# Performance work log

Measured on AMD Instinct MI355X. Metric: run time of the kernel, lower is better.

The kernel has to match this reference:

```python
import jax, jax.numpy as jnp
import numpy as np

B, C, T = 8, 128, 32768
OUT, K, DIL = 128, 2, 2


def dilated_indices(T, k, d):
    # Faithful vectorized version of the original Python double loop:
    # idx[span*k + j] = span + j*d, clamped to T (the zero-pad slot) when >= T+1.
    padded = T + 1
    idx = jnp.arange(padded)[:, None] + jnp.arange(k)[None, :] * d  # (padded, k)
    idx = idx.reshape(-1)                                           # (k*padded,)
    return jnp.where(idx >= padded, T, idx)


def setup_inputs() -> dict:
    key = jax.random.key(0)
    k1, k2, k3 = jax.random.split(key, 3)
    x = jax.random.normal(k1, (B, C, T), dtype=jnp.float32)
    # Conv1d(in=C, out=OUT, kernel_size=K) parameters
    W = jax.random.normal(k2, (OUT, C, K), dtype=jnp.float32) * 0.05
    b = jax.random.normal(k3, (OUT,), dtype=jnp.float32) * 0.05
    return {"x": x, "W": W, "b": b}


def reference(x, W, b):
    Bx, Cx, Tx = x.shape
    # pad one zero column at the end of the time axis (torch.cat with zeros)
    xp = jnp.concatenate([x, jnp.zeros((Bx, Cx, 1), x.dtype)], axis=2)  # (B,C,T+1)
    idx = dilated_indices(Tx, K, DIL)                                   # (K*(T+1),)
    swizzle = xp[:, :, idx]                                             # (B,C,K*(T+1))
    # Conv1d with stride == kernel_size over the swizzled buffer is a GEMM
    # over non-overlapping windows of size K.
    sw = swizzle.reshape(Bx, Cx, Tx + 1, K)                             # (B,C,T+1,K)
    out = jnp.einsum('bcpk,ock->bop', sw, W) + b[None, :, None]         # (B,OUT,T+1)
    return out
```

## Files before the change

kernel.cpp:

```cpp
#include <hip/hip_runtime.h>


namespace {

constexpr int kC   = 128;
constexpr int kT   = 32768;
constexpr int kP   = kT + 1;
constexpr int kOut = 128;
constexpr int kNP  = 128;
constexpr int kTilesPerB = kT / kNP;
constexpr int kUnitsPerBlock = 4;
constexpr int kNBlocks = 512;
constexpr int kLStride = 136;
constexpr int kLBuf    = 130 * kLStride;

typedef __attribute__((ext_vector_type(8))) short short8;
typedef __attribute__((ext_vector_type(4))) float f32x4;

__device__ __forceinline__ short f2bf(float f) {
    unsigned int u = __builtin_bit_cast(unsigned int, f);
    u += 0x7fffu + ((u >> 16) & 1u);
    return (short)(u >> 16);
}

__device__ __forceinline__ int lds_idx(int pos, int c) {
    return pos * kLStride + (c ^ (((pos >> 2) & 7) << 3));
}

__device__ __forceinline__ void lds_barrier() {
    asm volatile("s_waitcnt lgkmcnt(0)" ::: "memory");
    __builtin_amdgcn_s_barrier();
}

struct StageRegs {
    f32x4 m[16];
    float h[8];
};

__device__ __forceinline__ void stage_issue(const float* __restrict__ xb, int p0,
                                            int tid, StageRegs& r) {
    const int pgrp = tid & 31;
    const int cgrp = tid >> 5;
    const float* col = xb + p0 + pgrp * 4;
    #pragma unroll
    for (int j = 0; j < 16; ++j) {
        r.m[j] = *reinterpret_cast<const f32x4*>(col + ((size_t)(cgrp * 16 + j) << 15));
    }
    if (tid < 32) {
        const int gph = p0 + 128 + (tid & 1);
        const float* colh = xb + (gph < kT ? gph : 0);
        const int c0 = (tid >> 1) * 8;
        #pragma unroll
        for (int j = 0; j < 8; ++j) r.h[j] = colh[(size_t)(c0 + j) << 15];
    }
}

__device__ __forceinline__ void stage_commit(short* __restrict__ xs, int p0,
                                             int tid, const StageRegs& r) {
    const int pgrp = tid & 31;
    const int cgrp = tid >> 5;
    #pragma unroll
    for (int i = 0; i < 4; ++i) {
        const int pos = pgrp * 4 + i;
        #pragma unroll
        for (int h = 0; h < 2; ++h) {
            short8 v;
            #pragma unroll
            for (int j = 0; j < 8; ++j) v[j] = f2bf(r.m[h * 8 + j][i]);
            *reinterpret_cast<short8*>(xs + lds_idx(pos, cgrp * 16 + h * 8)) = v;
        }
    }
    if (tid < 32) {
        const int pos = 128 + (tid & 1);
        const bool okh = (p0 + pos) < kT;
        const int c0 = (tid >> 1) * 8;
        short8 v;
        #pragma unroll
        for (int j = 0; j < 8; ++j) v[j] = okh ? f2bf(r.h[j]) : (short)0;
        *reinterpret_cast<short8*>(xs + lds_idx(pos, c0)) = v;
    }
}

__global__ __launch_bounds__(256, 2) void dconv_mfma(
    const float* __restrict__ x, const float* __restrict__ W,
    const float* __restrict__ bias, float* __restrict__ out)
{
    __shared__ __align__(16) short xs[2][kLBuf];

    const int tid  = threadIdx.x;
    const int lane = tid & 63;
    const int wv   = tid >> 6;
    const int blk  = blockIdx.x;
    const int u0   = blk * kUnitsPerBlock;
    const int bb   = u0 >> 8;
    const int t0   = u0 & 255;

    if (blk < 8 && tid < kOut) {
        out[(size_t)blk * kOut * kP + (size_t)tid * kP + kT] = bias[tid];
    }

    const int rowbase = wv * 32;
    short8 wf[2][2][4];
    #pragma unroll
    for (int cc = 0; cc < 2; ++cc) {
        const int o = rowbase + cc * 16 + (lane & 15);
        #pragma unroll
        for (int s = 0; s < 4; ++s) {
            const int cb = s * 32 + (lane >> 4) * 8;
            const f32x4* wp = reinterpret_cast<const f32x4*>(W + o * (kC * 2) + cb * 2);
            f32x4 wr[4];
            #pragma unroll
            for (int q = 0; q < 4; ++q) wr[q] = wp[q];
            short8 f0, f1;
            #pragma unroll
            for (int q = 0; q < 4; ++q) {
                f0[q * 2 + 0] = f2bf(wr[q][0]);  f1[q * 2 + 0] = f2bf(wr[q][1]);
                f0[q * 2 + 1] = f2bf(wr[q][2]);  f1[q * 2 + 1] = f2bf(wr[q][3]);
            }
            wf[0][cc][s] = f0;
            wf[1][cc][s] = f1;
        }
    }
    const float bv0 = bias[rowbase + (lane & 15)];
    const float bv1 = bias[rowbase + 16 + (lane & 15)];

    const float* xb = x + (size_t)bb * kC * kT;
    float* ob = out + (size_t)bb * kOut * kP;

    StageRegs r;
    stage_issue(xb, t0 << 7, tid, r);
    stage_commit(xs[0], t0 << 7, tid, r);
    stage_issue(xb, (t0 + 1) << 7, tid, r);
    lds_barrier();

    #pragma unroll 1
    for (int i = 0; i < kUnitsPerBlock; ++i) {
        const short* cur = xs[i & 1];
        const int p0 = (t0 + i) << 7;

        f32x4 acc[2][8];
        #pragma unroll
        for (int nc = 0; nc < 8; ++nc) {
            #pragma unroll
            for (int rr = 0; rr < 4; ++rr) { acc[0][nc][rr] = bv0; acc[1][nc][rr] = bv1; }
        }
        #pragma unroll
        for (int tap = 0; tap < 2; ++tap) {
            #pragma unroll
            for (int s = 0; s < 4; ++s) {
                const int cb = s * 32 + (lane >> 4) * 8;
                #pragma unroll
                for (int nc = 0; nc < 8; ++nc) {
                    const int pos = nc * 16 + (lane & 15) + 2 * tap;
                    const short8 xf = *reinterpret_cast<const short8*>(cur + lds_idx(pos, cb));
                    acc[0][nc] = __builtin_amdgcn_mfma_f32_16x16x32_bf16(xf, wf[tap][0][s], acc[0][nc], 0, 0, 0);
                    acc[1][nc] = __builtin_amdgcn_mfma_f32_16x16x32_bf16(xf, wf[tap][1][s], acc[1][nc], 0, 0, 0);
                }
            }
        }

        if (i + 1 < kUnitsPerBlock) {
            stage_commit(xs[(i + 1) & 1], (t0 + i + 1) << 7, tid, r);
        }

        {
            const int o0   = rowbase + (lane & 15);
            const int prow = (lane >> 4) * 4;
            #pragma unroll
            for (int nc = 0; nc < 8; ++nc) {
                const int p = p0 + nc * 16 + prow;
                #pragma unroll
                for (int cc = 0; cc < 2; ++cc) {
                    __builtin_memcpy(ob + (size_t)(o0 + cc * 16) * kP + p, &acc[cc][nc],
                                     sizeof(f32x4));
                }
            }
        }

        if (i + 2 < kUnitsPerBlock) {
            stage_issue(xb, (t0 + i + 2) << 7, tid, r);
        }

        if (i + 1 < kUnitsPerBlock) lds_barrier();
    }
}

}

extern "C" void kernel_launch(void* const* d_in, const int* in_sizes, int n_in,
                              void* d_out, int out_size, void* d_ws, size_t ws_size,
                              hipStream_t stream) {
    const float* x    = (const float*)d_in[0];
    const float* W    = (const float*)d_in[1];
    const float* bias = (const float*)d_in[2];
    float* out        = (float*)d_out;

    dim3 grid(kNBlocks);
    dim3 block(256);
    hipLaunchKernelGGL(dconv_mfma, grid, block, 0, stream, x, W, bias, out);
}
```

Baseline: 305.6 us.

## Stage input tiles via direct global-to-LDS DMA with 64-position tiles

Replaces the register-staged global loads with global_load_lds DMA into an fp32 LDS staging buffer, then converts each tile to bf16 in LDS before the MFMA loop. Tiles shrink from 128 to 64 positions with 8 tiles per block, and a rotated write pattern avoids bank conflicts during conversion. The aim is to free the VGPRs that held staged data and overlap the next tile's DMA with compute. The cost is an extra LDS round trip and barrier per tile, and the bf16 buffer is now single-buffered.

```diff
diff --git a/kernel.cpp b/kernel.cpp
--- a/kernel.cpp
+++ b/kernel.cpp
@@ -7,14 +7,16 @@
 constexpr int kT   = 32768;
 constexpr int kP   = kT + 1;
 constexpr int kOut = 128;
-constexpr int kNP  = 128;
-constexpr int kTilesPerB = kT / kNP;
-constexpr int kUnitsPerBlock = 4;
+constexpr int kNP  = 64;
+constexpr int kTilesPerBatch = kT / kNP;
+constexpr int kTPB = 8;
 constexpr int kNBlocks = 512;
 constexpr int kLStride = 136;
-constexpr int kLBuf    = 130 * kLStride;
+constexpr int kF32Main = 128 * 64;
+constexpr int kF32Halo = 128 * 4;
 
 typedef __attribute__((ext_vector_type(8))) short short8;
+typedef __attribute__((ext_vector_type(4))) short s16x4;
 typedef __attribute__((ext_vector_type(4))) float f32x4;
 
 __device__ __forceinline__ short f2bf(float f) {
@@ -23,61 +25,74 @@
     return (short)(u >> 16);
 }
 
-__device__ __forceinline__ int lds_idx(int pos, int c) {
-    return pos * kLStride + (c ^ (((pos >> 2) & 7) << 3));
-}
-
+__device__ __forceinline__ void dma16(const float* g, float* l) {
+    __builtin_amdgcn_global_load_lds(
+        (const __attribute__((address_space(1))) void*)g,
+        (__attribute__((address_space(3))) void*)l,
+        16, 0, 0);
+}
+
+__device__ __forceinline__ void wait_vm0_barrier() {
+    asm volatile("s_waitcnt vmcnt(0)" ::: "memory");
+    __builtin_amdgcn_s_barrier();
+}
 __device__ __forceinline__ void lds_barrier() {
     asm volatile("s_waitcnt lgkmcnt(0)" ::: "memory");
     __builtin_amdgcn_s_barrier();
 }
 
-struct StageRegs {
-    f32x4 m[16];
-    float h[8];
-};
-
-__device__ __forceinline__ void stage_issue(const float* __restrict__ xb, int p0,
-                                            int tid, StageRegs& r) {
-    const int pgrp = tid & 31;
-    const int cgrp = tid >> 5;
-    const float* col = xb + p0 + pgrp * 4;
+__device__ __forceinline__ void stage_dma(const float* __restrict__ xb, int p0,
+                                          int wv, int lane, float* __restrict__ xf,
+                                          bool lastTile) {
+    const int q = lane >> 4;
+    const int s = lane & 15;
     #pragma unroll
-    for (int j = 0; j < 16; ++j) {
-        r.m[j] = *reinterpret_cast<const f32x4*>(col + ((size_t)(cgrp * 16 + j) << 15));
-    }
-    if (tid < 32) {
-        const int gph = p0 + 128 + (tid & 1);
-        const float* colh = xb + (gph < kT ? gph : 0);
-        const int c0 = (tid >> 1) * 8;
-        #pragma unroll
-        for (int j = 0; j < 8; ++j) r.h[j] = colh[(size_t)(c0 + j) << 15];
-    }
-}
-
-__device__ __forceinline__ void stage_commit(short* __restrict__ xs, int p0,
-                                             int tid, const StageRegs& r) {
-    const int pgrp = tid & 31;
-    const int cgrp = tid >> 5;
+    for (int jj = 0; jj < 8; ++jj) {
+        const int j  = wv * 8 + jj;
+        const int c  = 4 * j + q;
+        const int pw = (s - j) & 15;
+        dma16(xb + (size_t)c * kT + p0 + pw * 4, xf + j * 256);
+    }
+    if (wv == 0) {
+        #pragma unroll
+        for (int h = 0; h < 2; ++h) {
+            const int c  = 64 * h + lane;
+            const int gp = p0 + kNP;
+            dma16(xb + (size_t)c * kT + (lastTile ? p0 : gp),
+                  xf + kF32Main + h * 256);
+        }
+    }
+}
+
+__device__ __forceinline__ void convert_tile(const float* __restrict__ xf,
+                                             short* __restrict__ xs,
+                                             int tid, bool lastTile) {
+    const int cg = tid & 31;
+    const int c0 = cg * 4;
+    const int ph = tid >> 5;
     #pragma unroll
-    for (int i = 0; i < 4; ++i) {
-        const int pos = pgrp * 4 + i;
-        #pragma unroll
-        for (int h = 0; h < 2; ++h) {
-            short8 v;
-            #pragma unroll
-            for (int j = 0; j < 8; ++j) v[j] = f2bf(r.m[h * 8 + j][i]);
-            *reinterpret_cast<short8*>(xs + lds_idx(pos, cgrp * 16 + h * 8)) = v;
-        }
-    }
-    if (tid < 32) {
-        const int pos = 128 + (tid & 1);
-        const bool okh = (p0 + pos) < kT;
-        const int c0 = (tid >> 1) * 8;
-        short8 v;
-        #pragma unroll
-        for (int j = 0; j < 8; ++j) v[j] = okh ? f2bf(r.h[j]) : (short)0;
-        *reinterpret_cast<short8*>(xs + lds_idx(pos, c0)) = v;
+    for (int u = 0; u < 2; ++u) {
+        const int pw   = ph * 2 + u;
+        const int slot = (pw + cg) & 15;
+        f32x4 g[4];
+        #pragma unroll
+        for (int r = 0; r < 4; ++r) {
+            g[r] = *reinterpret_cast<const f32x4*>(xf + (c0 + r) * 64 + slot * 4);
+        }
+        #pragma unroll
+        for (int i = 0; i < 4; ++i) {
+            const int pos = pw * 4 + i;
+            s16x4 v;
+            v[0] = f2bf(g[0][i]); v[1] = f2bf(g[1][i]);
+            v[2] = f2bf(g[2][i]); v[3] = f2bf(g[3][i]);
+            *reinterpret_cast<s16x4*>(xs + pos * kLStride + c0) = v;
+        }
+    }
+    if (tid < 128) {
+        const int c = tid;
+        const f32x4 hh = *reinterpret_cast<const f32x4*>(xf + kF32Main + c * 4);
+        xs[64 * kLStride + c] = lastTile ? (short)0 : f2bf(hh[0]);
+        xs[65 * kLStride + c] = lastTile ? (short)0 : f2bf(hh[1]);
     }
 }
 
@@ -85,19 +100,24 @@
     const float* __restrict__ x, const float* __restrict__ W,
     const float* __restrict__ bias, float* __restrict__ out)
 {
-    __shared__ __align__(16) short xs[2][kLBuf];
+    __shared__ __align__(16) float xf[kF32Main + kF32Halo];
+    __shared__ __align__(16) short xs[66 * kLStride];
 
     const int tid  = threadIdx.x;
     const int lane = tid & 63;
     const int wv   = tid >> 6;
     const int blk  = blockIdx.x;
-    const int u0   = blk * kUnitsPerBlock;
-    const int bb   = u0 >> 8;
-    const int t0   = u0 & 255;
+    const int bb   = blk >> 6;
+    const int t0   = (blk & 63) * kTPB;
+
+    const float* xb = x + (size_t)bb * kC * kT;
+    float* ob = out + (size_t)bb * kOut * kP;
 
     if (blk < 8 && tid < kOut) {
         out[(size_t)blk * kOut * kP + (size_t)tid * kP + kT] = bias[tid];
     }
+
+    stage_dma(xb, t0 * kNP, wv, lane, xf, false);
 
     const int rowbase = wv * 32;
     short8 wf[2][2][4];
@@ -124,23 +144,24 @@
     const float bv0 = bias[rowbase + (lane & 15)];
     const float bv1 = bias[rowbase + 16 + (lane & 15)];
 
-    const float* xb = x + (size_t)bb * kC * kT;
-    float* ob = out + (size_t)bb * kOut * kP;
-
-    StageRegs r;
-    stage_issue(xb, t0 << 7, tid, r);
-    stage_commit(xs[0], t0 << 7, tid, r);
-    stage_issue(xb, (t0 + 1) << 7, tid, r);
-    lds_barrier();
+    wait_vm0_barrier();
 
     #pragma unroll 1
-    for (int i = 0; i < kUnitsPerBlock; ++i) {
-        const short* cur = xs[i & 1];
-        const int p0 = (t0 + i) << 7;
-
-        f32x4 acc[2][8];
-        #pragma unroll
-        for (int nc = 0; nc < 8; ++nc) {
+    for (int i = 0; i < kTPB; ++i) {
+        const int p0 = (t0 + i) * kNP;
+        const bool lastTile = (t0 + i) == (kTilesPerBatch - 1);
+
+        convert_tile(xf, xs, tid, lastTile);
+        lds_barrier();
+
+        if (i + 1 < kTPB) {
+            stage_dma(xb, (t0 + i + 1) * kNP, wv, lane, xf,
+                      (t0 + i + 1) == (kTilesPerBatch - 1));
+        }
+
+        f32x4 acc[2][4];
+        #pragma unroll
+        for (int nc = 0; nc < 4; ++nc) {
             #pragma unroll
             for (int rr = 0; rr < 4; ++rr) { acc[0][nc][rr] = bv0; acc[1][nc][rr] = bv1; }
         }
@@ -150,24 +171,20 @@
             for (int s = 0; s < 4; ++s) {
                 const int cb = s * 32 + (lane >> 4) * 8;
                 #pragma unroll
-                for (int nc = 0; nc < 8; ++nc) {
+                for (int nc = 0; nc < 4; ++nc) {
                     const int pos = nc * 16 + (lane & 15) + 2 * tap;
-                    const short8 xf = *reinterpret_cast<const short8*>(cur + lds_idx(pos, cb));
-                    acc[0][nc] = __builtin_amdgcn_mfma_f32_16x16x32_bf16(xf, wf[tap][0][s], acc[0][nc], 0, 0, 0);
-                    acc[1][nc] = __builtin_amdgcn_mfma_f32_16x16x32_bf16(xf, wf[tap][1][s], acc[1][nc], 0, 0, 0);
+                    const short8 xfrag = *reinterpret_cast<const short8*>(xs + pos * kLStride + cb);
+                    acc[0][nc] = __builtin_amdgcn_mfma_f32_16x16x32_bf16(xfrag, wf[tap][0][s], acc[0][nc], 0, 0, 0);
+                    acc[1][nc] = __builtin_amdgcn_mfma_f32_16x16x32_bf16(xfrag, wf[tap][1][s], acc[1][nc], 0, 0, 0);
                 }
             }
-        }
-
-        if (i + 1 < kUnitsPerBlock) {
-            stage_commit(xs[(i + 1) & 1], (t0 + i + 1) << 7, tid, r);
         }
 
         {
             const int o0   = rowbase + (lane & 15);
             const int prow = (lane >> 4) * 4;
             #pragma unroll
-            for (int nc = 0; nc < 8; ++nc) {
+            for (int nc = 0; nc < 4; ++nc) {
                 const int p = p0 + nc * 16 + prow;
                 #pragma unroll
                 for (int cc = 0; cc < 2; ++cc) {
@@ -177,11 +194,7 @@
             }
         }
 
-        if (i + 2 < kUnitsPerBlock) {
-            stage_issue(xb, (t0 + i + 2) << 7, tid, r);
-        }
-
-        if (i + 1 < kUnitsPerBlock) lds_barrier();
+        if (i + 1 < kTPB) wait_vm0_barrier();
     }
 }
 
```

Measured after the change: 290.2 us. 5.0% less time.

## Stage input via async global-to-LDS DMA ring and widen tiles to 256 positions

Applied to the files above, without the earlier changes.

Replaces the register-staged input load with global_load_lds DMA into a four-slot fp32 ring buffer of 16-channel chunks, kept three chunks ahead. Each chunk is then converted to bf16 in a single LDS tile. Blocks grow to 512 threads over 256-position tiles, with 8 waves split into 2 output groups by 4 position groups, and there are 256 blocks each doing 4 strided tiles. The goal is to cut VGPR pressure from staging and to overlap HBM reads with conversion. The cost is two barriers per chunk, serialized conversion and compute with no compute overlap within a tile, and a vmcnt(0) drain at the end of each tile.

```diff
diff --git a/kernel.cpp b/kernel.cpp
--- a/kernel.cpp
+++ b/kernel.cpp
@@ -7,12 +7,16 @@
 constexpr int kT   = 32768;
 constexpr int kP   = kT + 1;
 constexpr int kOut = 128;
-constexpr int kNP  = 128;
-constexpr int kTilesPerB = kT / kNP;
-constexpr int kUnitsPerBlock = 4;
-constexpr int kNBlocks = 512;
-constexpr int kLStride = 136;
-constexpr int kLBuf    = 130 * kLStride;
+constexpr int kTileP  = 256;
+constexpr int kTPB    = 4;
+constexpr int kGroups = 32;
+constexpr int kNBlocks = 8 * kGroups;
+constexpr int kChunks = 8;
+constexpr int kQ      = kTPB * kChunks;
+constexpr int kRowF   = 260;
+constexpr int kBufF   = 16 * kRowF + 64;
+constexpr int kPitch  = 136;
+constexpr int kXSRows = kTileP + 2;
 
 typedef __attribute__((ext_vector_type(8))) short short8;
 typedef __attribute__((ext_vector_type(4))) float f32x4;
@@ -23,90 +27,92 @@
     return (short)(u >> 16);
 }
 
-__device__ __forceinline__ int lds_idx(int pos, int c) {
-    return pos * kLStride + (c ^ (((pos >> 2) & 7) << 3));
-}
-
-__device__ __forceinline__ void lds_barrier() {
-    asm volatile("s_waitcnt lgkmcnt(0)" ::: "memory");
-    __builtin_amdgcn_s_barrier();
-}
-
-struct StageRegs {
-    f32x4 m[16];
-    float h[8];
-};
-
-__device__ __forceinline__ void stage_issue(const float* __restrict__ xb, int p0,
-                                            int tid, StageRegs& r) {
-    const int pgrp = tid & 31;
-    const int cgrp = tid >> 5;
-    const float* col = xb + p0 + pgrp * 4;
-    #pragma unroll
-    for (int j = 0; j < 16; ++j) {
-        r.m[j] = *reinterpret_cast<const f32x4*>(col + ((size_t)(cgrp * 16 + j) << 15));
-    }
-    if (tid < 32) {
-        const int gph = p0 + 128 + (tid & 1);
-        const float* colh = xb + (gph < kT ? gph : 0);
-        const int c0 = (tid >> 1) * 8;
-        #pragma unroll
-        for (int j = 0; j < 8; ++j) r.h[j] = colh[(size_t)(c0 + j) << 15];
-    }
-}
-
-__device__ __forceinline__ void stage_commit(short* __restrict__ xs, int p0,
-                                             int tid, const StageRegs& r) {
-    const int pgrp = tid & 31;
-    const int cgrp = tid >> 5;
-    #pragma unroll
-    for (int i = 0; i < 4; ++i) {
-        const int pos = pgrp * 4 + i;
-        #pragma unroll
-        for (int h = 0; h < 2; ++h) {
-            short8 v;
-            #pragma unroll
-            for (int j = 0; j < 8; ++j) v[j] = f2bf(r.m[h * 8 + j][i]);
-            *reinterpret_cast<short8*>(xs + lds_idx(pos, cgrp * 16 + h * 8)) = v;
-        }
-    }
-    if (tid < 32) {
-        const int pos = 128 + (tid & 1);
-        const bool okh = (p0 + pos) < kT;
-        const int c0 = (tid >> 1) * 8;
-        short8 v;
-        #pragma unroll
-        for (int j = 0; j < 8; ++j) v[j] = okh ? f2bf(r.h[j]) : (short)0;
-        *reinterpret_cast<short8*>(xs + lds_idx(pos, c0)) = v;
-    }
-}
-
-__global__ __launch_bounds__(256, 2) void dconv_mfma(
+__device__ __forceinline__ void dma16(const float* g, float* l) {
+    __builtin_amdgcn_global_load_lds(
+        (const __attribute__((address_space(1))) void*)g,
+        (__attribute__((address_space(3))) void*)l, 16, 0, 0);
+}
+__device__ __forceinline__ void dma4(const float* g, float* l) {
+    __builtin_amdgcn_global_load_lds(
+        (const __attribute__((address_space(1))) void*)g,
+        (__attribute__((address_space(3))) void*)l, 4, 0, 0);
+}
+
+__device__ __forceinline__ void issue_chunk(const float* __restrict__ xb, int p0,
+                                            int ch, float* __restrict__ buf,
+                                            int wv, int lane, bool last) {
+    #pragma unroll
+    for (int rr = 0; rr < 2; ++rr) {
+        const int r = 2 * wv + rr;
+        const int c = ch * 16 + r;
+        dma16(xb + (size_t)c * kT + p0 + lane * 4, buf + r * kRowF);
+    }
+    if (wv == 7) {
+        const int hc = ch * 16 + (lane >> 2);
+        const int hp = last ? p0 : (p0 + kTileP);
+        dma4(xb + (size_t)hc * kT + hp + (lane & 3), buf + 16 * kRowF);
+    }
+}
+
+__device__ __forceinline__ void convert_chunk(const float* __restrict__ buf,
+                                              short* __restrict__ xs,
+                                              int ch, int tid, bool last) {
+    const int c  = tid & 15;
+    const int pq = tid >> 4;
+    const int cc = ch * 16 + c;
+    #pragma unroll
+    for (int half = 0; half < 2; ++half) {
+        const int q = pq + half * 32;
+        const f32x4 v = *reinterpret_cast<const f32x4*>(buf + c * kRowF + q * 4);
+        #pragma unroll
+        for (int i = 0; i < 4; ++i) {
+            xs[(q * 4 + i) * kPitch + cc] = f2bf(v[i]);
+        }
+    }
+    if (tid < 16) {
+        const float h0 = buf[16 * kRowF + tid * 4 + 0];
+        const float h1 = buf[16 * kRowF + tid * 4 + 1];
+        xs[256 * kPitch + ch * 16 + tid] = last ? (short)0 : f2bf(h0);
+        xs[257 * kPitch + ch * 16 + tid] = last ? (short)0 : f2bf(h1);
+    }
+}
+
+#define WAIT_VM_CHUNKS()                                            \
+    do {                                                            \
+        if (wv == 7) asm volatile("s_waitcnt vmcnt(6)" ::: "memory"); \
+        else         asm volatile("s_waitcnt vmcnt(4)" ::: "memory"); \
+    } while (0)
+
+__global__ __launch_bounds__(512, 2) void dconv_mfma(
     const float* __restrict__ x, const float* __restrict__ W,
     const float* __restrict__ bias, float* __restrict__ out)
 {
-    __shared__ __align__(16) short xs[2][kLBuf];
+    __shared__ __align__(16) short xs[kXSRows * kPitch];
+    __shared__ __align__(16) float xf[4 * kBufF];
 
     const int tid  = threadIdx.x;
     const int lane = tid & 63;
     const int wv   = tid >> 6;
     const int blk  = blockIdx.x;
-    const int u0   = blk * kUnitsPerBlock;
-    const int bb   = u0 >> 8;
-    const int t0   = u0 & 255;
-
-    if (blk < 8 && tid < kOut) {
-        out[(size_t)blk * kOut * kP + (size_t)tid * kP + kT] = bias[tid];
-    }
-
-    const int rowbase = wv * 32;
-    short8 wf[2][2][4];
-    #pragma unroll
-    for (int cc = 0; cc < 2; ++cc) {
-        const int o = rowbase + cc * 16 + (lane & 15);
-        #pragma unroll
-        for (int s = 0; s < 4; ++s) {
-            const int cb = s * 32 + (lane >> 4) * 8;
+    const int bb   = blk >> 5;
+    const int g    = blk & 31;
+
+    const float* xb = x + (size_t)bb * kC * kT;
+    float* ob = out + (size_t)bb * kOut * kP;
+
+    if (g == 0 && tid < kOut) {
+        ob[(size_t)tid * kP + kT] = bias[tid];
+    }
+
+    const int ogrp = wv & 1;
+    const int pgrp = wv >> 1;
+    short8 wf[2][4][4];
+    #pragma unroll
+    for (int of = 0; of < 4; ++of) {
+        const int o = ogrp * 64 + of * 16 + (lane & 15);
+        #pragma unroll
+        for (int ks = 0; ks < 4; ++ks) {
+            const int cb = ks * 32 + (lane >> 4) * 8;
             const f32x4* wp = reinterpret_cast<const f32x4*>(W + o * (kC * 2) + cb * 2);
             f32x4 wr[4];
             #pragma unroll
@@ -117,71 +123,87 @@
                 f0[q * 2 + 0] = f2bf(wr[q][0]);  f1[q * 2 + 0] = f2bf(wr[q][1]);
                 f0[q * 2 + 1] = f2bf(wr[q][2]);  f1[q * 2 + 1] = f2bf(wr[q][3]);
             }
-            wf[0][cc][s] = f0;
-            wf[1][cc][s] = f1;
-        }
-    }
-    const float bv0 = bias[rowbase + (lane & 15)];
-    const float bv1 = bias[rowbase + 16 + (lane & 15)];
-
-    const float* xb = x + (size_t)bb * kC * kT;
-    float* ob = out + (size_t)bb * kOut * kP;
-
-    StageRegs r;
-    stage_issue(xb, t0 << 7, tid, r);
-    stage_commit(xs[0], t0 << 7, tid, r);
-    stage_issue(xb, (t0 + 1) << 7, tid, r);
-    lds_barrier();
+            wf[0][of][ks] = f0;
+            wf[1][of][ks] = f1;
+        }
+    }
+    float bv[4];
+    #pragma unroll
+    for (int of = 0; of < 4; ++of) bv[of] = bias[ogrp * 64 + of * 16 + (lane & 15)];
+
+    #pragma unroll
+    for (int q = 0; q < 3; ++q) {
+        const int tq = q >> 3, ch = q & 7;
+        const int p0 = (g + 32 * tq) * kTileP;
+        issue_chunk(xb, p0, ch, xf + (q & 3) * kBufF, wv, lane,
+                    (g == 31) && (tq == kTPB - 1));
+    }
 
     #pragma unroll 1
-    for (int i = 0; i < kUnitsPerBlock; ++i) {
-        const short* cur = xs[i & 1];
-        const int p0 = (t0 + i) << 7;
-
-        f32x4 acc[2][8];
-        #pragma unroll
-        for (int nc = 0; nc < 8; ++nc) {
-            #pragma unroll
-            for (int rr = 0; rr < 4; ++rr) { acc[0][nc][rr] = bv0; acc[1][nc][rr] = bv1; }
-        }
-        #pragma unroll
-        for (int tap = 0; tap < 2; ++tap) {
-            #pragma unroll
-            for (int s = 0; s < 4; ++s) {
-                const int cb = s * 32 + (lane >> 4) * 8;
+    for (int t = 0; t < kTPB; ++t) {
+        const int p0 = (g + 32 * t) * kTileP;
+        const bool lastT = (g == 31) && (t == kTPB - 1);
+
+        #pragma unroll 1
+        for (int j = 0; j < kChunks; ++j) {
+            const int q = t * kChunks + j;
+            WAIT_VM_CHUNKS();
+            __builtin_amdgcn_s_barrier();
+            convert_chunk(xf + (q & 3) * kBufF, xs, j, tid, lastT);
+            asm volatile("s_waitcnt lgkmcnt(0)" ::: "memory");
+            __builtin_amdgcn_s_barrier();
+            const int qn = q + 3;
+            if (qn < kQ) {
+                const int tq = qn >> 3, ch = qn & 7;
+                const int pn = (g + 32 * tq) * kTileP;
+                issue_chunk(xb, pn, ch, xf + (qn & 3) * kBufF, wv, lane,
+                            (g == 31) && (tq == kTPB - 1));
+            }
+        }
+
+        f32x4 acc[4][4];
+        #pragma unroll
+        for (int pf = 0; pf < 4; ++pf)
+            #pragma unroll
+            for (int of = 0; of < 4; ++of)
                 #pragma unroll
-                for (int nc = 0; nc < 8; ++nc) {
-                    const int pos = nc * 16 + (lane & 15) + 2 * tap;
-                    const short8 xf = *reinterpret_cast<const short8*>(cur + lds_idx(pos, cb));
-                    acc[0][nc] = __builtin_amdgcn_mfma_f32_16x16x32_bf16(xf, wf[tap][0][s], acc[0][nc], 0, 0, 0);
-                    acc[1][nc] = __builtin_amdgcn_mfma_f32_16x16x32_bf16(xf, wf[tap][1][s], acc[1][nc], 0, 0, 0);
+                for (int rr = 0; rr < 4; ++rr) acc[pf][of][rr] = bv[of];
+
+        #pragma unroll
+        for (int ks = 0; ks < 4; ++ks) {
+            const int cb = ks * 32 + (lane >> 4) * 8;
+            #pragma unroll
+            for (int tap = 0; tap < 2; ++tap) {
+                #pragma unroll
+                for (int pf = 0; pf < 4; ++pf) {
+                    const int pos = pgrp * 64 + pf * 16 + (lane & 15) + 2 * tap;
+                    const short8 xfr =
+                        *reinterpret_cast<const short8*>(xs + pos * kPitch + cb);
+                    #pragma unroll
+                    for (int of = 0; of < 4; ++of) {
+                        acc[pf][of] = __builtin_amdgcn_mfma_f32_16x16x32_bf16(
+                            xfr, wf[tap][of][ks], acc[pf][of], 0, 0, 0);
+                    }
                 }
             }
         }
 
-        if (i + 1 < kUnitsPerBlock) {
-            stage_commit(xs[(i + 1) & 1], (t0 + i + 1) << 7, tid, r);
-        }
-
         {
-            const int o0   = rowbase + (lane & 15);
-            const int prow = (lane >> 4) * 4;
-            #pragma unroll
-            for (int nc = 0; nc < 8; ++nc) {
-                const int p = p0 + nc * 16 + prow;
+            const int prow = pgrp * 64 + (lane >> 4) * 4;
+            const int o0   = ogrp * 64 + (lane & 15);
+            #pragma unroll
+            for (int pf = 0; pf < 4; ++pf) {
+                const int p = p0 + prow + pf * 16;
                 #pragma unroll
-                for (int cc = 0; cc < 2; ++cc) {
-                    __builtin_memcpy(ob + (size_t)(o0 + cc * 16) * kP + p, &acc[cc][nc],
-                                     sizeof(f32x4));
+                for (int of = 0; of < 4; ++of) {
+                    __builtin_memcpy(ob + (size_t)(o0 + of * 16) * kP + p,
+                                     &acc[pf][of], sizeof(f32x4));
                 }
             }
         }
 
-        if (i + 2 < kUnitsPerBlock) {
-            stage_issue(xb, (t0 + i + 2) << 7, tid, r);
-        }
-
-        if (i + 1 < kUnitsPerBlock) lds_barrier();
+        asm volatile("s_waitcnt vmcnt(0)" ::: "memory");
+        __builtin_amdgcn_s_barrier();
     }
 }
 
@@ -196,6 +218,6 @@
     float* out        = (float*)d_out;
 
     dim3 grid(kNBlocks);
-    dim3 block(256);
+    dim3 block(512);
     hipLaunchKernelGGL(dconv_mfma, grid, block, 0, stream, x, W, bias, out);
 }
```

New measurement: 297.3 us. -2.7%, faster.
